# Kernel tuning notes

Measured on AMD Instinct MI355X. Metric: run time of the kernel, lower is better.

The kernel has to match this reference:

```python
import jax, jax.numpy as jnp
import numpy as np

K = (3, 5, 7)
TAU_MIN, TAU_MAX = 0.03, 0.5


def _l2norm(x, axis=1, eps=1e-12):
    # matches torch F.normalize: x / max(||x||, eps)
    n = jnp.sqrt(jnp.sum(x * x, axis=axis, keepdims=True))
    return x / jnp.maximum(n, eps)


def _affinity_one(feat, kappa_ch, qw_k, kw_k, k):
    # feat: (B, C, H, W); kappa_ch: (B, 1, H, W); qw_k/kw_k: (Ca, C)
    B, C, H, W = feat.shape
    q = jnp.einsum('bchw,oc->bohw', feat, qw_k)
    key = jnp.einsum('bchw,oc->bohw', feat, kw_k)
    qn = _l2norm(q)
    kn = _l2norm(key)
    p = k // 2
    knp = jnp.pad(kn, ((0, 0), (0, 0), (p, p), (p, p)))
    # windowed cosine correlation: loop over the small fixed set of k*k offsets
    sims = []
    for dy in range(k):
        for dx in range(k):
            sims.append(jnp.sum(qn * knp[:, :, dy:dy + H, dx:dx + W], axis=1))
    sim = jnp.stack(sims, axis=1)  # (B, k*k, H, W)
    # temperature from curvature: GLOBAL min/max over the sliced channel
    kmin = kappa_ch.min()
    kmax = kappa_ch.max()
    kap_n = (kappa_ch - kmin) / (kmax - kmin + 1e-06)
    tau = jnp.clip(TAU_MAX - kap_n * (TAU_MAX - TAU_MIN), TAU_MIN, TAU_MAX)
    return sim / (tau + 1e-06)  # broadcast (B,kk,H,W) / (B,1,H,W)


def setup_inputs() -> dict:
    key = jax.random.key(0)
    k1, k2, k3, k4 = jax.random.split(key, 4)
    B, C, H, W = 4, 64, 256, 256
    CA = 32
    feat = jax.random.normal(k1, (B, C, H, W), dtype=jnp.float32)
    kappa = jax.random.uniform(k2, (B, len(K), H, W), dtype=jnp.float32)
    scale = 1.0 / np.sqrt(C)
    qw = jax.random.normal(k3, (len(K), CA, C), dtype=jnp.float32) * scale
    kw = jax.random.normal(k4, (len(K), CA, C), dtype=jnp.float32) * scale
    return {'feat': feat, 'kappa': kappa, 'qw': qw, 'kw': kw}


def reference(feat, kappa, qw, kw):
    out = []
    for i, k in enumerate(K):
        out.append(_affinity_one(feat, kappa[:, i:i + 1], qw[i], kw[i], k))
    return tuple(out)
```

## Files before the change

kernel.cpp:

```cpp
#include <hip/hip_runtime.h>
#include <stdint.h>

#define HW   65536
#define IMG  256
#define NB   4
#define NC   64
#define NA   32

typedef __attribute__((ext_vector_type(8))) short short8v;
typedef __attribute__((ext_vector_type(4))) float f32x4;

__device__ __forceinline__ unsigned short f2bf(float x) {
  unsigned u = __float_as_uint(x);
  u += 0x7FFFu + ((u >> 16) & 1u);
  return (unsigned short)(u >> 16);
}
__device__ __forceinline__ float bfval(unsigned short h) { return __uint_as_float((unsigned)h << 16); }
__device__ __forceinline__ unsigned packbf(float a, float b) {
  return (unsigned)f2bf(a) | ((unsigned)f2bf(b) << 16);
}

__global__ void prep_afrag(const float* __restrict__ qw, const float* __restrict__ kw,
                           unsigned short* __restrict__ afrag, unsigned* __restrict__ mm) {
  int idx = blockIdx.x * 256 + threadIdx.x;
  if (blockIdx.x == 0 && threadIdx.x < 6)
    mm[threadIdx.x] = (threadIdx.x < 3) ? 0xFFFFFFFFu : 0u;
  if (idx >= 3 * 4 * 2 * 2 * 64 * 8) return;
  int j    = idx & 7;
  int lane = (idx >> 3) & 63;
  int h    = (idx >> 9) & 1;
  int ks   = (idx >> 10) & 1;
  int mt   = (idx >> 11) & 3;
  int i    = idx >> 13;
  int s = mt >> 1;
  int o = (mt & 1) * 16 + (lane & 15);
  int c = ks * 32 + (lane >> 4) * 8 + j;
  float v = (s ? kw : qw)[((size_t)i * NA + o) * NC + c];
  unsigned short hi = f2bf(v);
  afrag[idx] = h ? f2bf(v - bfval(hi)) : hi;
}

__global__ __launch_bounds__(256) void minmax_k(const float* __restrict__ kappa,
                                                unsigned* __restrict__ mm) {
  const int i = blockIdx.y;
  const unsigned* ku = (const unsigned*)kappa;
  unsigned lo = 0xFFFFFFFFu, hi = 0u;
  for (int idx = blockIdx.x * 256 + threadIdx.x; idx < NB * HW; idx += gridDim.x * 256) {
    int b = idx >> 16, p = idx & (HW - 1);
    unsigned v = ku[((size_t)(b * 3 + i)) * HW + p];
    lo = min(lo, v); hi = max(hi, v);
  }
#pragma unroll
  for (int d = 32; d >= 1; d >>= 1) {
    lo = min(lo, (unsigned)__shfl_xor((int)lo, d, 64));
    hi = max(hi, (unsigned)__shfl_xor((int)hi, d, 64));
  }
  __shared__ unsigned slo[4], shi[4];
  if ((threadIdx.x & 63) == 0) { slo[threadIdx.x >> 6] = lo; shi[threadIdx.x >> 6] = hi; }
  __syncthreads();
  if (threadIdx.x == 0) {
    lo = min(min(slo[0], slo[1]), min(slo[2], slo[3]));
    hi = max(max(shi[0], shi[1]), max(shi[2], shi[3]));
    atomicMin(&mm[i], lo);
    atomicMax(&mm[i + 3], hi);
  }
}

__global__ __launch_bounds__(256) void proj_all(const float* __restrict__ feat,
                                                const unsigned short* __restrict__ afr,
                                                unsigned* __restrict__ qb,
                                                unsigned* __restrict__ kb,
                                                const int nsl, const int i0) {
  const int t = blockIdx.x;
  const int b = t >> 8;
  const int p0 = (t & 255) * 256;
  const int lane = threadIdx.x & 63;
  const int w = threadIdx.x >> 6;
  const int pbase = p0 + w * 64;

  short8v bh[4][2], bl[4][2];
  const float* fb = feat + (size_t)b * NC * HW;
#pragma unroll
  for (int ks = 0; ks < 2; ++ks) {
    float fv[32];
#pragma unroll
    for (int nt = 0; nt < 4; ++nt) {
      const int px = pbase + nt * 16 + (lane & 15);
      const float* fp = fb + (size_t)(ks * 32 + (lane >> 4) * 8) * HW + px;
#pragma unroll
      for (int j = 0; j < 8; ++j) fv[nt * 8 + j] = fp[(size_t)j * HW];
    }
#pragma unroll
    for (int nt = 0; nt < 4; ++nt)
#pragma unroll
      for (int j = 0; j < 8; ++j) {
        float f = fv[nt * 8 + j];
        unsigned short h = f2bf(f);
        bh[nt][ks][j] = (short)h;
        bl[nt][ks][j] = (short)f2bf(f - bfval(h));
      }
  }

#pragma unroll 1
  for (int sl = 0; sl < nsl; ++sl) {
#pragma unroll 1
    for (int s = 0; s < 2; ++s) {
      const unsigned short* af = afr + (size_t)(i0 + sl) * 8192;

      short8v ah[2][2], al[2][2];
#pragma unroll
      for (int m = 0; m < 2; ++m)
#pragma unroll
        for (int ks = 0; ks < 2; ++ks) {
          int mt = s * 2 + m;
          const unsigned short* base = af + (size_t)((mt * 2 + ks) * 2) * 512 + lane * 8;
          ah[m][ks] = *(const short8v*)(base);
          al[m][ks] = *(const short8v*)(base + 512);
        }

      f32x4 acc[2][4];
#pragma unroll
      for (int m = 0; m < 2; ++m)
#pragma unroll
        for (int nt = 0; nt < 4; ++nt) acc[m][nt] = (f32x4){0.f, 0.f, 0.f, 0.f};

#pragma unroll
      for (int nt = 0; nt < 4; ++nt)
#pragma unroll
        for (int ks = 0; ks < 2; ++ks)
#pragma unroll
          for (int m = 0; m < 2; ++m) {
            acc[m][nt] = __builtin_amdgcn_mfma_f32_16x16x32_bf16(ah[m][ks], bh[nt][ks], acc[m][nt], 0, 0, 0);
            acc[m][nt] = __builtin_amdgcn_mfma_f32_16x16x32_bf16(ah[m][ks], bl[nt][ks], acc[m][nt], 0, 0, 0);
            acc[m][nt] = __builtin_amdgcn_mfma_f32_16x16x32_bf16(al[m][ks], bh[nt][ks], acc[m][nt], 0, 0, 0);
          }

      unsigned* dstbuf = (s ? kb : qb) + (size_t)sl * NB * HW * 16;
#pragma unroll
      for (int nt = 0; nt < 4; ++nt) {
        float ssq = 0.f;
#pragma unroll
        for (int m = 0; m < 2; ++m)
#pragma unroll
          for (int r = 0; r < 4; ++r) ssq = fmaf(acc[m][nt][r], acc[m][nt][r], ssq);
        ssq += __shfl_xor(ssq, 16, 64);
        ssq += __shfl_xor(ssq, 32, 64);
        float inv = 1.0f / fmaxf(sqrtf(ssq), 1e-12f);
        const int px = pbase + nt * 16 + (lane & 15);
        const size_t pix = (size_t)b * HW + px;
#pragma unroll
        for (int m = 0; m < 2; ++m) {
          int c0 = m * 16 + (lane >> 4) * 4;
          uint2 v;
          v.x = packbf(acc[m][nt][0] * inv, acc[m][nt][1] * inv);
          v.y = packbf(acc[m][nt][2] * inv, acc[m][nt][3] * inv);
          *(uint2*)(dstbuf + pix * 16 + (c0 >> 1)) = v;
        }
      }
    }
  }
}

template <int KS>
__device__ __forceinline__ void corr_mfma_body(float* Csh,
                                               const unsigned* __restrict__ qn,
                                               const unsigned* __restrict__ kn,
                                               const float* __restrict__ kappa,
                                               const unsigned* __restrict__ mm,
                                               const int i, const int b,
                                               float* __restrict__ out) {
  constexpr int P = KS / 2;
  constexpr int KK = KS * KS;
  const int y0 = blockIdx.y * 16, x0 = blockIdx.x * 16;
  const int lane = threadIdx.x & 63, w = threadIdx.x >> 6;
  const int cq = lane & 15;
  const int rq = lane >> 4;
  const int y = y0 + w * 4 + rq;
  const int x = x0 + cq;

  float* Cw = Csh + w * 2592;

  short8v A[4];
#pragma unroll
  for (int yl = 0; yl < 4; ++yl) {
    const unsigned* p = qn + ((size_t)b * HW + (size_t)(y0 + w * 4 + yl) * IMG + x0 + cq) * 16 + rq * 4;
    A[yl] = *(const short8v*)p;
  }

  float kap = kappa[((size_t)(b * 3 + i)) * HW + (size_t)y * IMG + x];
  float kmin = __uint_as_float(mm[i]);
  float kmax = __uint_as_float(mm[i + 3]);
  float kapn = (kap - kmin) / (kmax - kmin + 1e-6f);
  float tau = fminf(fmaxf(0.5f - kapn * (0.5f - 0.03f), 0.03f), 0.5f);
  float scale = 1.0f / (tau + 1e-6f);

  const int kx0 = x0 - P + cq;
  const int kx1 = kx0 + 16;

#pragma unroll 1
  for (int dy = 0; dy < KS; ++dy) {
    asm volatile("s_waitcnt lgkmcnt(0)" ::: "memory");
#pragma unroll
    for (int yl = 0; yl < 4; ++yl) {
      const int ky = y0 + w * 4 + yl + dy - P;
      f32x4 a0 = {0.f, 0.f, 0.f, 0.f}, a1 = {0.f, 0.f, 0.f, 0.f};
      if ((unsigned)ky < (unsigned)IMG) {
        const unsigned* krow = kn + ((size_t)b * HW + (size_t)ky * IMG) * 16;
        short8v B0 = {0, 0, 0, 0, 0, 0, 0, 0};
        short8v B1 = {0, 0, 0, 0, 0, 0, 0, 0};
        if ((unsigned)kx0 < (unsigned)IMG) B0 = *(const short8v*)(krow + (size_t)kx0 * 16 + rq * 4);
        if ((unsigned)kx1 < (unsigned)IMG) B1 = *(const short8v*)(krow + (size_t)kx1 * 16 + rq * 4);
        a0 = __builtin_amdgcn_mfma_f32_16x16x32_bf16(A[yl], B0, a0, 0, 0, 0);
        a1 = __builtin_amdgcn_mfma_f32_16x16x32_bf16(A[yl], B1, a1, 0, 0, 0);
      }
      *(f32x4*)(Cw + yl * 648 + cq * 20 + rq * 4) = a0;
      *(f32x4*)(Cw + yl * 648 + (16 + cq) * 20 + rq * 4) = a1;
    }
    asm volatile("s_waitcnt lgkmcnt(0)" ::: "memory");
    __builtin_amdgcn_sched_barrier(0);
    float* ob = out + ((size_t)b * KK + (size_t)dy * KS) * HW + (size_t)y * IMG + x;
#pragma unroll
    for (int dx = 0; dx < KS; ++dx) {
      float v = Cw[rq * 648 + (cq + dx) * 20 + cq];
      ob[(size_t)dx * HW] = v * scale;
    }
  }
}

__global__ __launch_bounds__(256) void corr_all(const unsigned* __restrict__ qb,
                                                const unsigned* __restrict__ kb,
                                                const float* __restrict__ kappa,
                                                const unsigned* __restrict__ mm,
                                                const int i0, float* __restrict__ out) {
  __shared__ __align__(16) float Csh[10368];
  const int sl = blockIdx.z >> 2;
  const int b = blockIdx.z & 3;
  const int i = i0 + sl;
  const unsigned* qn = qb + (size_t)sl * NB * HW * 16;
  const unsigned* kn = kb + (size_t)sl * NB * HW * 16;
  const size_t plane = (size_t)NB * HW;
  if (i == 0)
    corr_mfma_body<3>(Csh, qn, kn, kappa, mm, 0, b, out);
  else if (i == 1)
    corr_mfma_body<5>(Csh, qn, kn, kappa, mm, 1, b, out + plane * 9);
  else
    corr_mfma_body<7>(Csh, qn, kn, kappa, mm, 2, b, out + plane * 34);
}

extern "C" void kernel_launch(void* const* d_in, const int* in_sizes, int n_in,
                              void* d_out, int out_size, void* d_ws, size_t ws_size,
                              hipStream_t stream) {
  const float* feat  = (const float*)d_in[0];
  const float* kappa = (const float*)d_in[1];
  const float* qw    = (const float*)d_in[2];
  const float* kw    = (const float*)d_in[3];
  float* out = (float*)d_out;

  char* ws = (char*)d_ws;
  unsigned* mm = (unsigned*)ws;
  unsigned short* afrag = (unsigned short*)(ws + 64);
  unsigned* qbuf = (unsigned*)(ws + 65536);

  const size_t slot = (size_t)NB * HW * 16;
  const size_t need3 = 65536 + (size_t)6 * slot * 4;
  const int fused = (ws_size >= need3) ? 1 : 0;
  const int nsl = fused ? 3 : 1;
  unsigned* kbuf = qbuf + (size_t)nsl * slot;

  hipLaunchKernelGGL(prep_afrag, dim3(96), dim3(256), 0, stream, qw, kw, afrag, mm);
  hipLaunchKernelGGL(minmax_k, dim3(64, 3), dim3(256), 0, stream, kappa, mm);

  if (fused) {
    hipLaunchKernelGGL(proj_all, dim3(NB * HW / 256), dim3(256), 0, stream,
                       feat, afrag, qbuf, kbuf, 3, 0);
    hipLaunchKernelGGL(corr_all, dim3(IMG / 16, IMG / 16, NB * 3), dim3(256), 0, stream,
                       qbuf, kbuf, kappa, mm, 0, out);
  } else {
    for (int i = 0; i < 3; ++i) {
      hipLaunchKernelGGL(proj_all, dim3(NB * HW / 256), dim3(256), 0, stream,
                         feat, afrag, qbuf, kbuf, 1, i);
      hipLaunchKernelGGL(corr_all, dim3(IMG / 16, IMG / 16, NB), dim3(256), 0, stream,
                         qbuf, kbuf, kappa, mm, i, out);
    }
  }
}
```

Before: 115.6 us.

## Coalesce projection stores via LDS, double-buffer key loads, reverse slice order in corr

The projection kernel now stages normalized bf16 q/k fragments in shared memory and writes them out as contiguous 16-byte rows, replacing scattered 8-byte global stores. The correlation kernel fully unrolls the dy loop and prefetches the next row's key fragments into a second register buffer while computing the current one. The LDS scratch tile shrinks to 22 columns, and the corr grid mapping processes the largest window first when fused. The prefetch raises register pressure, and the launch host code (not shown) must match the new slot mapping.

```diff
diff --git a/kernel.cpp b/kernel.cpp
--- a/kernel.cpp
+++ b/kernel.cpp
@@ -71,12 +71,14 @@
                                                 unsigned* __restrict__ qb,
                                                 unsigned* __restrict__ kb,
                                                 const int nsl, const int i0) {
+  __shared__ __align__(16) unsigned Psh[4 * 64 * 20];
   const int t = blockIdx.x;
   const int b = t >> 8;
   const int p0 = (t & 255) * 256;
   const int lane = threadIdx.x & 63;
   const int w = threadIdx.x >> 6;
   const int pbase = p0 + w * 64;
+  unsigned* Pw = Psh + w * (64 * 20);
 
   short8v bh[4][2], bl[4][2];
   const float* fb = feat + (size_t)b * NC * HW;
@@ -135,7 +137,7 @@
             acc[m][nt] = __builtin_amdgcn_mfma_f32_16x16x32_bf16(al[m][ks], bh[nt][ks], acc[m][nt], 0, 0, 0);
           }
 
-      unsigned* dstbuf = (s ? kb : qb) + (size_t)sl * NB * HW * 16;
+      asm volatile("" ::: "memory");
 #pragma unroll
       for (int nt = 0; nt < 4; ++nt) {
         float ssq = 0.f;
@@ -146,16 +148,23 @@
         ssq += __shfl_xor(ssq, 16, 64);
         ssq += __shfl_xor(ssq, 32, 64);
         float inv = 1.0f / fmaxf(sqrtf(ssq), 1e-12f);
-        const int px = pbase + nt * 16 + (lane & 15);
-        const size_t pix = (size_t)b * HW + px;
+        const int pxl = nt * 16 + (lane & 15);
 #pragma unroll
         for (int m = 0; m < 2; ++m) {
-          int c0 = m * 16 + (lane >> 4) * 4;
           uint2 v;
           v.x = packbf(acc[m][nt][0] * inv, acc[m][nt][1] * inv);
           v.y = packbf(acc[m][nt][2] * inv, acc[m][nt][3] * inv);
-          *(uint2*)(dstbuf + pix * 16 + (c0 >> 1)) = v;
+          *(uint2*)(Pw + pxl * 20 + m * 8 + (lane >> 4) * 2) = v;
         }
+      }
+      asm volatile("s_waitcnt lgkmcnt(0)" ::: "memory");
+      __builtin_amdgcn_sched_barrier(0);
+      unsigned* dst = ((s ? kb : qb) + (size_t)sl * NB * HW * 16) +
+                      ((size_t)b * HW + pbase) * 16;
+#pragma unroll
+      for (int r = 0; r < 4; ++r) {
+        uint4 v = *(const uint4*)(Pw + (r * 16 + (lane >> 2)) * 20 + (lane & 3) * 4);
+        *(uint4*)(dst + r * 256 + lane * 4) = v;
       }
     }
   }
@@ -171,14 +180,16 @@
                                                float* __restrict__ out) {
   constexpr int P = KS / 2;
   constexpr int KK = KS * KS;
+  constexpr int CST = 20;
+  constexpr int NCOL = 22;
+  constexpr int YST = NCOL * CST;
   const int y0 = blockIdx.y * 16, x0 = blockIdx.x * 16;
   const int lane = threadIdx.x & 63, w = threadIdx.x >> 6;
   const int cq = lane & 15;
   const int rq = lane >> 4;
   const int y = y0 + w * 4 + rq;
   const int x = x0 + cq;
-
-  float* Cw = Csh + w * 2592;
+  float* Cw = Csh + w * (4 * YST);
 
   short8v A[4];
 #pragma unroll
@@ -196,32 +207,45 @@
 
   const int kx0 = x0 - P + cq;
   const int kx1 = kx0 + 16;
-
-#pragma unroll 1
+  const int kyb = y0 + w * 4 - P;
+  const unsigned* knb = kn + (size_t)b * HW * 16;
+
+  short8v B0[2][4], B1[2][4];
+  auto loadB = [&](int dy, int buf) {
+#pragma unroll
+    for (int yl = 0; yl < 4; ++yl) {
+      const int ky = kyb + yl + dy;
+      short8v z = {0, 0, 0, 0, 0, 0, 0, 0};
+      B0[buf][yl] = z; B1[buf][yl] = z;
+      if ((unsigned)ky < (unsigned)IMG) {
+        const unsigned* krow = knb + (size_t)ky * IMG * 16;
+        if ((unsigned)kx0 < (unsigned)IMG) B0[buf][yl] = *(const short8v*)(krow + (size_t)kx0 * 16 + rq * 4);
+        if ((unsigned)kx1 < (unsigned)IMG) B1[buf][yl] = *(const short8v*)(krow + (size_t)kx1 * 16 + rq * 4);
+      }
+    }
+  };
+  loadB(0, 0);
+
+#pragma unroll
   for (int dy = 0; dy < KS; ++dy) {
-    asm volatile("s_waitcnt lgkmcnt(0)" ::: "memory");
+    const int cur = dy & 1, nxt = cur ^ 1;
+    if (dy + 1 < KS) loadB(dy + 1, nxt);
+    asm volatile("" ::: "memory");
 #pragma unroll
     for (int yl = 0; yl < 4; ++yl) {
-      const int ky = y0 + w * 4 + yl + dy - P;
       f32x4 a0 = {0.f, 0.f, 0.f, 0.f}, a1 = {0.f, 0.f, 0.f, 0.f};
-      if ((unsigned)ky < (unsigned)IMG) {
-        const unsigned* krow = kn + ((size_t)b * HW + (size_t)ky * IMG) * 16;
-        short8v B0 = {0, 0, 0, 0, 0, 0, 0, 0};
-        short8v B1 = {0, 0, 0, 0, 0, 0, 0, 0};
-        if ((unsigned)kx0 < (unsigned)IMG) B0 = *(const short8v*)(krow + (size_t)kx0 * 16 + rq * 4);
-        if ((unsigned)kx1 < (unsigned)IMG) B1 = *(const short8v*)(krow + (size_t)kx1 * 16 + rq * 4);
-        a0 = __builtin_amdgcn_mfma_f32_16x16x32_bf16(A[yl], B0, a0, 0, 0, 0);
-        a1 = __builtin_amdgcn_mfma_f32_16x16x32_bf16(A[yl], B1, a1, 0, 0, 0);
-      }
-      *(f32x4*)(Cw + yl * 648 + cq * 20 + rq * 4) = a0;
-      *(f32x4*)(Cw + yl * 648 + (16 + cq) * 20 + rq * 4) = a1;
+      a0 = __builtin_amdgcn_mfma_f32_16x16x32_bf16(A[yl], B0[cur][yl], a0, 0, 0, 0);
+      a1 = __builtin_amdgcn_mfma_f32_16x16x32_bf16(A[yl], B1[cur][yl], a1, 0, 0, 0);
+      *(f32x4*)(Cw + yl * YST + cq * CST + rq * 4) = a0;
+      if (cq < NCOL - 16)
+        *(f32x4*)(Cw + yl * YST + (16 + cq) * CST + rq * 4) = a1;
     }
     asm volatile("s_waitcnt lgkmcnt(0)" ::: "memory");
     __builtin_amdgcn_sched_barrier(0);
     float* ob = out + ((size_t)b * KK + (size_t)dy * KS) * HW + (size_t)y * IMG + x;
 #pragma unroll
     for (int dx = 0; dx < KS; ++dx) {
-      float v = Cw[rq * 648 + (cq + dx) * 20 + cq];
+      float v = Cw[rq * YST + (cq + dx) * CST + cq];
       ob[(size_t)dx * HW] = v * scale;
     }
   }
@@ -232,12 +256,14 @@
                                                 const float* __restrict__ kappa,
                                                 const unsigned* __restrict__ mm,
                                                 const int i0, float* __restrict__ out) {
-  __shared__ __align__(16) float Csh[10368];
-  const int sl = blockIdx.z >> 2;
+  __shared__ __align__(16) float Csh[7040];
+  const int g = blockIdx.z >> 2;
   const int b = blockIdx.z & 3;
-  const int i = i0 + sl;
-  const unsigned* qn = qb + (size_t)sl * NB * HW * 16;
-  const unsigned* kn = kb + (size_t)sl * NB * HW * 16;
+  const int fused = (gridDim.z > 4) ? 1 : 0;
+  const int i = fused ? (2 - g) : i0;
+  const int slot = fused ? i : 0;
+  const unsigned* qn = qb + (size_t)slot * NB * HW * 16;
+  const unsigned* kn = kb + (size_t)slot * NB * HW * 16;
   const size_t plane = (size_t)NB * HW;
   if (i == 0)
     corr_mfma_body<3>(Csh, qn, kn, kappa, mm, 0, b, out);
```

Result: slower. 123.9 us (+7.2%).
